# Kernel tuning notes

Hardware: AMD Instinct MI355X
Metric: run time of the kernel (lower is better)

## Reference

```python
import jax, jax.numpy as jnp
import numpy as np

H = 768       # hidden size
NH = 12       # num attention heads
DH = H // NH  # head dim = 64
B = 32
S = 512


def setup_inputs() -> dict:
    key = jax.random.key(0)
    ks = jax.random.split(key, 7)
    scale = 1.0 / np.sqrt(H)
    return {
        "inputs": jax.random.normal(ks[0], (B, S, H), dtype=jnp.float32),
        "Wq": jax.random.normal(ks[1], (H, H), dtype=jnp.float32) * scale,
        "bq": jnp.zeros((H,), dtype=jnp.float32),
        "Wk": jax.random.normal(ks[2], (H, H), dtype=jnp.float32) * scale,
        "bk": jnp.zeros((H,), dtype=jnp.float32),
        "Wv": jax.random.normal(ks[3], (H, H), dtype=jnp.float32) * scale,
        "bv": jnp.zeros((H,), dtype=jnp.float32),
    }


def reference(inputs, Wq, bq, Wk, bk, Wv, bv):
    # BertSelfAttention: linear projections (torch Linear: x @ W.T + b)
    def split_heads(x):  # [B,S,H] -> [B,NH,S,DH]
        return x.reshape(B, S, NH, DH).transpose(0, 2, 1, 3)

    q = split_heads(inputs @ Wq.T + bq)
    k = split_heads(inputs @ Wk.T + bk)
    v = split_heads(inputs @ Wv.T + bv)

    # scores [B,NH,S,S]; the wrapper adds an all-zero attention mask (no-op)
    scores = jnp.einsum("bhqd,bhkd->bhqk", q, k) / jnp.sqrt(jnp.float32(DH))
    probs = jax.nn.softmax(scores, axis=-1)
    ctx = jnp.einsum("bhqk,bhkd->bhqd", probs, v)  # [B,NH,S,DH]
    ctx = ctx.transpose(0, 2, 1, 3).reshape(B, S, H)
    return jnp.tanh(ctx)
```

## Files before the change

### kernel.cpp

```cpp
#include <hip/hip_runtime.h>
#include <hip/hip_bf16.h>
#include <cmath>

#define Bc   32
#define Sc_  512
#define Hc   768
#define NHc  12
#define DHc  64
#define Mc   (Bc * Sc_)
#define Ntot (3 * Hc)

#define QSCALE 0.18033688011112042f

typedef __attribute__((ext_vector_type(8))) short short8v;
typedef __attribute__((ext_vector_type(8))) unsigned short ushort8v;
typedef __attribute__((ext_vector_type(4))) float f32x4;

static __device__ __forceinline__ ushort f2b(float f) {
    __hip_bfloat16 h = __float2bfloat16(f);
    return *reinterpret_cast<ushort*>(&h);
}
static __device__ __forceinline__ ushort2 f2b2(float a, float b) {
    __hip_bfloat162 h = __float22bfloat162_rn(float2{a, b});
    return *reinterpret_cast<ushort2*>(&h);
}

static __device__ __forceinline__ void gl2lds(const ushort* g, ushort* l) {
    __builtin_amdgcn_global_load_lds(
        (const __attribute__((address_space(1))) unsigned int*)g,
        (__attribute__((address_space(3))) unsigned int*)l, 16, 0, 0);
}

static __device__ __forceinline__ float fast_tanh(float x) {
    float e = __builtin_amdgcn_exp2f(x * 2.885390081777927f);
    return 1.0f - 2.0f * __builtin_amdgcn_rcpf(e + 1.0f);
}

__global__ __launch_bounds__(256) void convert_pack(
    const float* __restrict__ X,
    const float* __restrict__ Wq, const float* __restrict__ Wk,
    const float* __restrict__ Wv,
    const float* __restrict__ bq, const float* __restrict__ bk,
    const float* __restrict__ bv,
    ushort* __restrict__ Xt, ushort* __restrict__ Wt, float* __restrict__ bbp)
{
    const int bx = blockIdx.x;
    const int panel = bx / 12, kcg = bx % 12;
    const int t = threadIdx.x;

    const float* base;
    ushort* out;
    if (panel < 128) {
        base = X + (size_t)panel * 128 * Hc;
        out  = Xt + (size_t)panel * (96 * 1024);
    } else {
        int nblk = panel - 128;
        int n0 = nblk * 128;
        int z = n0 / Hc;
        int nn0 = n0 - z * Hc;
        const float* W = (z == 0) ? Wq : (z == 1) ? Wk : Wv;
        base = W + (size_t)nn0 * Hc;
        out  = Wt + (size_t)nblk * (96 * 1024);
    }

    #pragma unroll
    for (int v = 0; v < 4; ++v) {
        int idx  = v * 256 + t;
        int row  = idx & 127;
        int kc_l = idx >> 7;
        int kc   = kcg * 8 + kc_l;
        const float* p = base + (size_t)row * Hc + kc * 8;
        float4 f0 = *(const float4*)&p[0];
        float4 f1 = *(const float4*)&p[4];
        ushort2 h0 = f2b2(f0.x, f0.y);
        ushort2 h1 = f2b2(f0.z, f0.w);
        ushort2 h2 = f2b2(f1.x, f1.y);
        ushort2 h3 = f2b2(f1.z, f1.w);
        ushort8v o;
        o[0] = h0.x; o[1] = h0.y; o[2] = h1.x; o[3] = h1.y;
        o[4] = h2.x; o[5] = h2.y; o[6] = h3.x; o[7] = h3.y;
        *(ushort8v*)&out[(size_t)kc * 1024 + row * 8] = o;
    }

    if (bx == 0) {
        for (int i = t; i < Ntot; i += 256) {
            int z = i / Hc, nn = i - z * Hc;
            bbp[i] = ((z == 0) ? bq : (z == 1) ? bk : bv)[nn];
        }
    }
}

__global__ __launch_bounds__(256) void qkv_mfma(
    const ushort* __restrict__ Xt, const ushort* __restrict__ Wt,
    const float* __restrict__ bbp,
    ushort* __restrict__ Qb, ushort* __restrict__ Kt, ushort* __restrict__ Vt)
{
    const int tid = threadIdx.x;
    const int wave = tid >> 6, lane = tid & 63;
    const int quad = lane >> 4, l16 = lane & 15;
    const int wr = wave >> 1, wc = wave & 1;
    const int m0 = blockIdx.x * 128;
    const int n0 = blockIdx.y * 128;

    __shared__ __align__(16) ushort As[4096];
    __shared__ __align__(16) ushort Bs[4096];

    f32x4 acc[4][4];
    #pragma unroll
    for (int i = 0; i < 4; ++i)
        #pragma unroll
        for (int j = 0; j < 4; ++j) acc[i][j] = (f32x4)(0.f);

    const ushort* gA = Xt + (size_t)blockIdx.x * (96 * 1024) + wave * 1024 + lane * 8;
    const ushort* gB = Wt + (size_t)blockIdx.y * (96 * 1024) + wave * 1024 + lane * 8;
    ushort* lA = As + wave * 1024;
    ushort* lB = Bs + wave * 1024;

    for (int t = 0; t < 24; ++t) {
        const ushort* ga = gA + t * 4096;
        const ushort* gb = gB + t * 4096;
        gl2lds(ga,       lA);
        gl2lds(ga + 512, lA + 512);
        gl2lds(gb,       lB);
        gl2lds(gb + 512, lB + 512);
        __syncthreads();

        short8v a[4], b[4];
        #pragma unroll
        for (int i = 0; i < 4; ++i)
            a[i] = *(const short8v*)&As[quad * 1024 + (wr * 64 + i * 16 + l16) * 8];
        #pragma unroll
        for (int j = 0; j < 4; ++j)
            b[j] = *(const short8v*)&Bs[quad * 1024 + (wc * 64 + j * 16 + l16) * 8];
        #pragma unroll
        for (int i = 0; i < 4; ++i)
            #pragma unroll
            for (int j = 0; j < 4; ++j)
                acc[i][j] = __builtin_amdgcn_mfma_f32_16x16x32_bf16(
                    a[i], b[j], acc[i][j], 0, 0, 0);
        __syncthreads();
    }

    const int z = n0 / Hc;
    #pragma unroll
    for (int j = 0; j < 4; ++j) {
        const int n  = n0 + wc * 64 + j * 16 + l16;
        const int nn = n - z * Hc;
        const int h  = nn >> 6, d = nn & 63;
        const float bias = bbp[n];
        #pragma unroll
        for (int i = 0; i < 4; ++i) {
            const int mbase = m0 + wr * 64 + i * 16 + quad * 4;
            const int bb = mbase >> 9;
            const int s0 = mbase & 511;
            const size_t head = (size_t)(bb * NHc + h) * (Sc_ * DHc);
            if (z == 0) {
                size_t base = head + (size_t)s0 * DHc + d;
                #pragma unroll
                for (int r = 0; r < 4; ++r)
                    Qb[base + (size_t)r * DHc] = f2b((acc[i][j][r] + bias) * QSCALE);
            } else if (z == 1) {
                size_t base = head + (s0 >> 6) * 4096 + (d >> 3) * 512
                            + (s0 & 63) * 8 + (d & 7);
                #pragma unroll
                for (int r = 0; r < 4; ++r)
                    Kt[base + r * 8] = f2b(acc[i][j][r] + bias);
            } else {
                size_t base = head + (s0 >> 6) * 4096 + ((s0 & 63) >> 3) * 512
                            + d * 8 + (s0 & 7);
                ushort4 o;
                o.x = f2b(acc[i][j][0] + bias);
                o.y = f2b(acc[i][j][1] + bias);
                o.z = f2b(acc[i][j][2] + bias);
                o.w = f2b(acc[i][j][3] + bias);
                *(ushort4*)&Vt[base] = o;
            }
        }
    }
}

__global__ __launch_bounds__(256) void attn_mfma(
    const ushort* __restrict__ Qb, const ushort* __restrict__ Kt,
    const ushort* __restrict__ Vt, float* __restrict__ out)
{
    const int bid = blockIdx.x;
    const int super = bid >> 5, l = bid & 31;
    const int head_lin = super * 8 + (l & 7);
    const int qt = l >> 3;
    const int b = head_lin / NHc, h = head_lin % NHc;

    const int wave = threadIdx.x >> 6;
    const int lane = threadIdx.x & 63;
    const int quad = lane >> 4, l16 = lane & 15;
    const int q0 = qt * 128 + wave * 32;
    const int sw = l16 & 7;

    const size_t head = (size_t)head_lin * (Sc_ * DHc);
    const ushort* __restrict__ Q = Qb + head;
    const ushort* __restrict__ K = Kt + head;
    const ushort* __restrict__ V = Vt + head;

    __shared__ __align__(16) ushort Plds[4][2][1024];

    short8v aq[2][2];
    #pragma unroll
    for (int u = 0; u < 2; ++u)
        #pragma unroll
        for (int hf = 0; hf < 2; ++hf)
            aq[u][hf] = *(const short8v*)
                &Q[(size_t)(q0 + u * 16 + l16) * DHc + hf * 32 + quad * 8];

    short8v ones;
    #pragma unroll
    for (int i = 0; i < 8; ++i) ones[i] = (short)0x3F80;

    f32x4 o[2][4], rsum[2];
    #pragma unroll
    for (int u = 0; u < 2; ++u) {
        rsum[u] = (f32x4)(0.f);
        #pragma unroll
        for (int t = 0; t < 4; ++t) o[u][t] = (f32x4)(0.f);
    }

    for (int kb = 0; kb < 8; ++kb) {
        const ushort* Kb_ = K + kb * 4096;
        const ushort* Vb_ = V + kb * 4096;

        short8v kf[4][2];
        #pragma unroll
        for (int t = 0; t < 4; ++t) {
            kf[t][0] = *(const short8v*)&Kb_[quad * 512 + (t * 16 + l16) * 8];
            kf[t][1] = *(const short8v*)&Kb_[(4 + quad) * 512 + (t * 16 + l16) * 8];
        }

        f32x4 sa[2][4];
        #pragma unroll
        for (int u = 0; u < 2; ++u)
            #pragma unroll
            for (int t = 0; t < 4; ++t) {
                f32x4 s = __builtin_amdgcn_mfma_f32_16x16x32_bf16(
                    kf[t][0], aq[u][0], (f32x4)(0.f), 0, 0, 0);
                sa[u][t] = __builtin_amdgcn_mfma_f32_16x16x32_bf16(
                    kf[t][1], aq[u][1], s, 0, 0, 0);
            }

        #pragma unroll
        for (int u = 0; u < 2; ++u) {
            #pragma unroll
            for (int t = 0; t < 4; ++t) {
                float p0 = __builtin_amdgcn_exp2f(sa[u][t][0]);
                float p1 = __builtin_amdgcn_exp2f(sa[u][t][1]);
                float p2 = __builtin_amdgcn_exp2f(sa[u][t][2]);
                float p3 = __builtin_amdgcn_exp2f(sa[u][t][3]);
                ushort2 lo = f2b2(p0, p1);
                ushort2 hi = f2b2(p2, p3);
                ushort4 pk;
                pk.x = lo.x; pk.y = lo.y; pk.z = hi.x; pk.w = hi.y;
                int c = t * 2 + (quad >> 1);
                int addr = l16 * 64 + ((c ^ sw) * 8) + (quad & 1) * 4;
                *(ushort4*)&Plds[wave][u][addr] = pk;
            }
        }

        short8v pa[2][2];
        #pragma unroll
        for (int u = 0; u < 2; ++u) {
            pa[u][0] = *(const short8v*)&Plds[wave][u][l16 * 64 + ((quad ^ sw) * 8)];
            pa[u][1] = *(const short8v*)&Plds[wave][u][l16 * 64 + (((4 + quad) ^ sw) * 8)];
        }

        #pragma unroll
        for (int u = 0; u < 2; ++u) {
            rsum[u] = __builtin_amdgcn_mfma_f32_16x16x32_bf16(
                pa[u][0], ones, rsum[u], 0, 0, 0);
            rsum[u] = __builtin_amdgcn_mfma_f32_16x16x32_bf16(
                pa[u][1], ones, rsum[u], 0, 0, 0);
        }

        #pragma unroll
        for (int t2 = 0; t2 < 4; ++t2) {
            short8v vf0 = *(const short8v*)&Vb_[quad * 512 + (t2 * 16 + l16) * 8];
            short8v vf1 = *(const short8v*)&Vb_[(4 + quad) * 512 + (t2 * 16 + l16) * 8];
            #pragma unroll
            for (int u = 0; u < 2; ++u) {
                o[u][t2] = __builtin_amdgcn_mfma_f32_16x16x32_bf16(
                    pa[u][0], vf0, o[u][t2], 0, 0, 0);
                o[u][t2] = __builtin_amdgcn_mfma_f32_16x16x32_bf16(
                    pa[u][1], vf1, o[u][t2], 0, 0, 0);
            }
        }
    }

    #pragma unroll
    for (int u = 0; u < 2; ++u) {
        #pragma unroll
        for (int r = 0; r < 4; ++r) {
            float inv = __builtin_amdgcn_rcpf(rsum[u][r]);
            int q = q0 + u * 16 + quad * 4 + r;
            size_t base = ((size_t)b * Sc_ + q) * Hc + h * DHc;
            #pragma unroll
            for (int t2 = 0; t2 < 4; ++t2)
                out[base + t2 * 16 + l16] = fast_tanh(o[u][t2][r] * inv);
        }
    }
}

extern "C" void kernel_launch(void* const* d_in, const int* in_sizes, int n_in,
                              void* d_out, int out_size, void* d_ws, size_t ws_size,
                              hipStream_t stream) {
    const float* X  = (const float*)d_in[0];
    const float* Wq = (const float*)d_in[1];
    const float* bq = (const float*)d_in[2];
    const float* Wk = (const float*)d_in[3];
    const float* bk = (const float*)d_in[4];
    const float* Wv = (const float*)d_in[5];
    const float* bv = (const float*)d_in[6];
    float* out = (float*)d_out;

    ushort* Qb  = (ushort*)d_ws;
    ushort* Kt  = Qb + (size_t)Mc * Hc;
    ushort* Vt  = Kt + (size_t)Mc * Hc;
    ushort* Xt  = Vt + (size_t)Mc * Hc;
    ushort* Wt  = Xt + (size_t)Mc * Hc;
    float*  bbp = (float*)(Wt + (size_t)Ntot * Hc);

    convert_pack<<<dim3(1752), 256, 0, stream>>>(
        X, Wq, Wk, Wv, bq, bk, bv, Xt, Wt, bbp);

    dim3 g1(Mc / 128, Ntot / 128);
    qkv_mfma<<<g1, 256, 0, stream>>>(Xt, Wt, bbp, Qb, Kt, Vt);

    attn_mfma<<<dim3(1536), 256, 0, stream>>>(Qb, Kt, Vt, out);
}
```

Before: 230.5 us.

## Stage fp32-to-bf16 packing through LDS and hoist V loads in attention loop

The conversion kernel now reads each row with coalesced float4 loads across 16 threads into a padded shared-memory tile, then writes the packed k-chunk layout from LDS. Before this, each thread read 32-byte strided row segments. The attention kernel now loads V fragments together with K fragments at the top of each key block and unrolls the key loop by two, so global load latency overlaps with the score MFMAs and softmax. The cost is extra LDS use and a barrier in the packing kernel, plus higher register pressure in attention, which could reduce occupancy.

Result: slower. 235.7 us (+2.3%).

```diff
diff --git a/kernel.cpp b/kernel.cpp
--- a/kernel.cpp
+++ b/kernel.cpp
@@ -47,6 +47,8 @@
     const int bx = blockIdx.x;
     const int panel = bx / 12, kcg = bx % 12;
     const int t = threadIdx.x;
+
+    __shared__ ushort T[128][68];
 
     const float* base;
     ushort* out;
@@ -62,24 +64,32 @@
         base = W + (size_t)nn0 * Hc;
         out  = Wt + (size_t)nblk * (96 * 1024);
     }
-
-    #pragma unroll
-    for (int v = 0; v < 4; ++v) {
-        int idx  = v * 256 + t;
-        int row  = idx & 127;
-        int kc_l = idx >> 7;
-        int kc   = kcg * 8 + kc_l;
-        const float* p = base + (size_t)row * Hc + kc * 8;
-        float4 f0 = *(const float4*)&p[0];
-        float4 f1 = *(const float4*)&p[4];
-        ushort2 h0 = f2b2(f0.x, f0.y);
-        ushort2 h1 = f2b2(f0.z, f0.w);
-        ushort2 h2 = f2b2(f1.x, f1.y);
-        ushort2 h3 = f2b2(f1.z, f1.w);
+    const int k0 = kcg * 64;
+
+    const int slot = t & 15, rsub = t >> 4;
+    #pragma unroll
+    for (int rnd = 0; rnd < 8; ++rnd) {
+        int row = rnd * 16 + rsub;
+        const float* p = base + (size_t)row * Hc + k0 + slot * 4;
+        float4 f = *(const float4*)p;
+        ushort2 h0 = f2b2(f.x, f.y);
+        ushort2 h1 = f2b2(f.z, f.w);
+        ushort4 u;
+        u.x = h0.x; u.y = h0.y; u.z = h1.x; u.w = h1.y;
+        *(ushort4*)&T[row][slot * 4] = u;
+    }
+    __syncthreads();
+
+    const int row_w = t & 127, kh = t >> 7;
+    #pragma unroll
+    for (int rnd = 0; rnd < 4; ++rnd) {
+        int kc_l = rnd * 2 + kh;
+        ushort4 lo = *(const ushort4*)&T[row_w][kc_l * 8];
+        ushort4 hi = *(const ushort4*)&T[row_w][kc_l * 8 + 4];
         ushort8v o;
-        o[0] = h0.x; o[1] = h0.y; o[2] = h1.x; o[3] = h1.y;
-        o[4] = h2.x; o[5] = h2.y; o[6] = h3.x; o[7] = h3.y;
-        *(ushort8v*)&out[(size_t)kc * 1024 + row * 8] = o;
+        o[0] = lo.x; o[1] = lo.y; o[2] = lo.z; o[3] = lo.w;
+        o[4] = hi.x; o[5] = hi.y; o[6] = hi.z; o[7] = hi.w;
+        *(ushort8v*)&out[(size_t)(kcg * 8 + kc_l) * 1024 + row_w * 8] = o;
     }
 
     if (bx == 0) {
@@ -222,15 +232,18 @@
         for (int t = 0; t < 4; ++t) o[u][t] = (f32x4)(0.f);
     }
 
+    #pragma unroll 2
     for (int kb = 0; kb < 8; ++kb) {
         const ushort* Kb_ = K + kb * 4096;
         const ushort* Vb_ = V + kb * 4096;
 
-        short8v kf[4][2];
+        short8v kf[4][2], vf[4][2];
         #pragma unroll
         for (int t = 0; t < 4; ++t) {
             kf[t][0] = *(const short8v*)&Kb_[quad * 512 + (t * 16 + l16) * 8];
             kf[t][1] = *(const short8v*)&Kb_[(4 + quad) * 512 + (t * 16 + l16) * 8];
+            vf[t][0] = *(const short8v*)&Vb_[quad * 512 + (t * 16 + l16) * 8];
+            vf[t][1] = *(const short8v*)&Vb_[(4 + quad) * 512 + (t * 16 + l16) * 8];
         }
 
         f32x4 sa[2][4];
@@ -278,17 +291,14 @@
         }
 
         #pragma unroll
-        for (int t2 = 0; t2 < 4; ++t2) {
-            short8v vf0 = *(const short8v*)&Vb_[quad * 512 + (t2 * 16 + l16) * 8];
-            short8v vf1 = *(const short8v*)&Vb_[(4 + quad) * 512 + (t2 * 16 + l16) * 8];
+        for (int t2 = 0; t2 < 4; ++t2)
             #pragma unroll
             for (int u = 0; u < 2; ++u) {
                 o[u][t2] = __builtin_amdgcn_mfma_f32_16x16x32_bf16(
-                    pa[u][0], vf0, o[u][t2], 0, 0, 0);
+                    pa[u][0], vf[t2][0], o[u][t2], 0, 0, 0);
                 o[u][t2] = __builtin_amdgcn_mfma_f32_16x16x32_bf16(
-                    pa[u][1], vf1, o[u][t2], 0, 0, 0);
+                    pa[u][1], vf[t2][1], o[u][t2], 0, 0, 0);
             }
-        }
     }
 
     #pragma unroll
```
